# Kernel optimization log

Hardware: AMD Instinct MI355X
Metric: run time of the kernel (lower is better)

Reference implementation:

```python
import jax, jax.numpy as jnp
import numpy as np

DIM = 384
HEADS = 6
DIM_HEAD = 64
INNER = HEADS * DIM_HEAD  # 384


def setup_inputs() -> dict:
    key = jax.random.key(0)
    ks = jax.random.split(key, 6)
    s = 0.02
    return {
        "x_q": jax.random.normal(ks[0], (8, 4096, DIM), dtype=jnp.float32),
        "x_kv": jax.random.normal(ks[1], (8, 4096, DIM), dtype=jnp.float32),
        "Wq": jax.random.normal(ks[2], (DIM, INNER), dtype=jnp.float32) * s,
        "Wkv": jax.random.normal(ks[3], (DIM, 2 * INNER), dtype=jnp.float32) * s,
        "Wout": jax.random.normal(ks[4], (INNER, DIM), dtype=jnp.float32) * s,
        "bout": jax.random.normal(ks[5], (DIM,), dtype=jnp.float32) * s,
    }


def _split_heads(t, b, n):
    # [b, n, h*d] -> [b, h, n, d]
    return t.reshape(b, n, HEADS, DIM_HEAD).transpose(0, 2, 1, 3)


def reference(x_q, x_kv, Wq, Wkv, Wout, bout):
    b, nq, _ = x_q.shape
    nkv = x_kv.shape[1]
    q = x_q @ Wq                      # [b, nq, inner]
    kv_proj = x_kv @ Wkv              # [b, nkv, 2*inner]
    k, v = jnp.split(kv_proj, 2, axis=-1)
    q = _split_heads(q, b, nq)        # [b, h, nq, d]
    k = _split_heads(k, b, nkv)       # [b, h, nkv, d]
    v = _split_heads(v, b, nkv)       # [b, h, nkv, d]
    q = jax.nn.elu(q) + 1.0
    k = jax.nn.elu(k) + 1.0
    kv = jnp.einsum('bhnd,bhnm->bhdm', k, v)             # [b, h, d, d]
    z = 1.0 / (jnp.einsum('bhnd,bhd->bhn', q, k.sum(axis=2)) + 1e-6)
    out = jnp.einsum('bhnd,bhdm->bhnm', q, kv) * z[..., None]  # [b, h, nq, d]
    out = out.transpose(0, 2, 1, 3).reshape(b, nq, INNER)
    return out @ Wout + bout
```

## Files before the change

### kernel.cpp

```cpp
#include <hip/hip_runtime.h>
#include <math.h>

#define BATCH 8
#define SEQ 4096
#define DIMSZ 384
#define HEADS 6
#define DH 64
#define MTOT (BATCH * SEQ)
#define KD 384

typedef short short8 __attribute__((ext_vector_type(8)));
typedef float floatx4 __attribute__((ext_vector_type(4)));
typedef unsigned short ushort4v __attribute__((ext_vector_type(4)));
typedef unsigned short ushort8v __attribute__((ext_vector_type(8)));

__device__ __forceinline__ float elu1(float x) { return x > 0.f ? x + 1.f : __expf(x); }

__device__ __forceinline__ unsigned short f2b(float f) {
    unsigned int u = __float_as_uint(f);
    u = (u + 0x7fffu + ((u >> 16) & 1u)) >> 16;
    return (unsigned short)u;
}
__device__ __forceinline__ float b2f(unsigned short u) {
    return __uint_as_float(((unsigned int)u) << 16);
}

__device__ __forceinline__ void gl16(const void* g, void* l) {
    __builtin_amdgcn_global_load_lds((const __attribute__((address_space(1))) unsigned int*)g,
                                     (__attribute__((address_space(3))) unsigned int*)l, 16, 0, 0);
}

__global__ __launch_bounds__(256) void conv_x2(const float* __restrict__ xq,
                                               const float* __restrict__ xkv,
                                               unsigned short* __restrict__ dq,
                                               unsigned short* __restrict__ dkv) {
    int bx = blockIdx.x;
    const float* src;
    unsigned short* dst;
    if (bx < 6144) { src = xkv; dst = dkv; }
    else { src = xq; dst = dq; bx -= 6144; }
    size_t i = ((size_t)bx * 256 + threadIdx.x) * 8;
    float4 a = *(const float4*)&src[i];
    float4 b = *(const float4*)&src[i + 4];
    ushort8v o;
    o[0] = f2b(a.x); o[1] = f2b(a.y); o[2] = f2b(a.z); o[3] = f2b(a.w);
    o[4] = f2b(b.x); o[5] = f2b(b.y); o[6] = f2b(b.z); o[7] = f2b(b.w);
    *(ushort8v*)&dst[i] = o;
}

__global__ __launch_bounds__(256) void conv_wt3(const float* __restrict__ Wq,
                                                const float* __restrict__ Wkv,
                                                const float* __restrict__ Wout,
                                                unsigned short* __restrict__ WqT,
                                                unsigned short* __restrict__ WkvT,
                                                unsigned short* __restrict__ WoutT) {
    __shared__ float tile[32][33];
    int bx = blockIdx.x;
    const float* W;
    unsigned short* WT;
    int N;
    if (bx < 12) { W = Wq; WT = WqT; N = DIMSZ; }
    else if (bx < 36) { W = Wkv; WT = WkvT; N = 2 * DIMSZ; bx -= 12; }
    else { W = Wout; WT = WoutT; N = DIMSZ; bx -= 36; }
    const int n0 = bx * 32, k0 = blockIdx.y * 32;
    const int tx = threadIdx.x & 31, ty = threadIdx.x >> 5;
#pragma unroll
    for (int i = 0; i < 32; i += 8) tile[ty + i][tx] = W[(size_t)(k0 + ty + i) * N + n0 + tx];
    __syncthreads();
#pragma unroll
    for (int i = 0; i < 32; i += 8)
        WT[(size_t)(n0 + ty + i) * KD + k0 + tx] = f2b(tile[tx][ty + i]);
}

__global__ __launch_bounds__(256, 4) void gemm_kv(const unsigned short* __restrict__ A,
                                                  const unsigned short* __restrict__ WkvT,
                                                  float* __restrict__ pkv,
                                                  float* __restrict__ pks) {
    __shared__ __align__(16) unsigned short buf[17408];
    __shared__ float ksLDS[128];
    unsigned short* As = buf;
    unsigned short* Bs = buf + 8192;
    const int tid = threadIdx.x;
    const int lane = tid & 63, wave = tid >> 6;
    const int l15 = lane & 15, qd = lane >> 4;
    const int fid = blockIdx.x;
    const int xcd = fid & 7;
    const int s = fid >> 3;
    const int h = s % HEADS;
    const int rtl = s / HEADS;
    const int row0 = (xcd * 32 + rtl) * 128;
    const int pidx = (xcd * HEADS + h) * 32 + rtl;
    const int wm = (wave & 1) * 64, wn = (wave >> 1) * 64;

    const unsigned short* Ab = A + (size_t)row0 * KD;
    const unsigned short* Bb = WkvT + (size_t)(h * DH) * KD;
    const int srow = tid >> 3;
    const int scol = (((tid & 7) ^ (srow & 7)) * 8);

    floatx4 zero = {0.f, 0.f, 0.f, 0.f};
    floatx4 acc[4][4];
#pragma unroll
    for (int i = 0; i < 4; ++i)
#pragma unroll
        for (int j = 0; j < 4; ++j) acc[i][j] = zero;

    const int sw = l15 & 7;
    for (int kk = 0; kk < KD; kk += 64) {
        __syncthreads();
#pragma unroll
        for (int i = 0; i < 4; ++i)
            gl16(Ab + (size_t)(i * 32 + srow) * KD + kk + scol, As + i * 2048 + wave * 512);
#pragma unroll
        for (int i = 0; i < 4; ++i)
            gl16(Bb + (size_t)(i * 32 + srow + (i >= 2 ? 320 : 0)) * KD + kk + scol,
                 Bs + i * 2048 + wave * 512);
        __syncthreads();
#pragma unroll
        for (int t = 0; t < 2; ++t) {
            const int chnk = ((t * 4 + qd) ^ sw) * 8;
            short8 af[4], bfr[4];
#pragma unroll
            for (int mi = 0; mi < 4; ++mi)
                af[mi] = *(const short8*)&As[(wm + mi * 16 + l15) * 64 + chnk];
#pragma unroll
            for (int ni = 0; ni < 4; ++ni)
                bfr[ni] = *(const short8*)&Bs[(wn + ni * 16 + l15) * 64 + chnk];
#pragma unroll
            for (int mi = 0; mi < 4; ++mi)
#pragma unroll
                for (int ni = 0; ni < 4; ++ni)
                    acc[mi][ni] = __builtin_amdgcn_mfma_f32_16x16x32_bf16(af[mi], bfr[ni],
                                                                          acc[mi][ni], 0, 0, 0);
        }
    }

    __syncthreads();
    const bool kw = (wn == 0);
    float ksp[4] = {};
#pragma unroll
    for (int mi = 0; mi < 4; ++mi)
#pragma unroll
        for (int ni = 0; ni < 4; ++ni) {
            const int rb = wm + mi * 16 + qd * 4;
            const int cl = wn + ni * 16 + l15;
            ushort4v o;
#pragma unroll
            for (int r = 0; r < 4; ++r) {
                float v = acc[mi][ni][r];
                if (kw) { v = elu1(v); ksp[ni] += v; }
                o[r] = f2b(v);
            }
            *(ushort4v*)&buf[cl * 136 + rb] = o;
        }
    if (kw) {
#pragma unroll
        for (int ni = 0; ni < 4; ++ni) {
            float v = ksp[ni];
            v += __shfl_xor(v, 16);
            v += __shfl_xor(v, 32);
            if (lane < 16) ksLDS[wave * 64 + ni * 16 + lane] = v;
        }
    }
    __syncthreads();
    floatx4 kva[4];
#pragma unroll
    for (int j = 0; j < 4; ++j) kva[j] = zero;
#pragma unroll
    for (int nk = 0; nk < 4; ++nk) {
        short8 afk = *(const short8*)&buf[(wave * 16 + l15) * 136 + nk * 32 + qd * 8];
#pragma unroll
        for (int nj = 0; nj < 4; ++nj) {
            short8 bfv = *(const short8*)&buf[(64 + nj * 16 + l15) * 136 + nk * 32 + qd * 8];
            kva[nj] = __builtin_amdgcn_mfma_f32_16x16x32_bf16(afk, bfv, kva[nj], 0, 0, 0);
        }
    }
    float* P = pkv + (size_t)pidx * 4096;
#pragma unroll
    for (int nj = 0; nj < 4; ++nj)
#pragma unroll
        for (int r = 0; r < 4; ++r)
            __builtin_nontemporal_store(kva[nj][r],
                                        &P[(wave * 16 + qd * 4 + r) * 64 + nj * 16 + l15]);
    if (tid < 64)
        __builtin_nontemporal_store(ksLDS[tid] + ksLDS[64 + tid], &pks[pidx * 64 + tid]);
}

__global__ __launch_bounds__(256) void kv_reduce(const float* __restrict__ pkv,
                                                 const float* __restrict__ pks,
                                                 unsigned short* __restrict__ kv_bf,
                                                 float* __restrict__ ksum_g) {
    const int bh = blockIdx.x;
    const int tid = threadIdx.x;
    unsigned short* kb = kv_bf + (size_t)bh * 4096;
    for (int i0 = tid * 4; i0 < 4096; i0 += 1024) {
        float4 sum = {0.f, 0.f, 0.f, 0.f};
#pragma unroll
        for (int c = 0; c < 32; ++c) {
            float4 p = *(const float4*)&pkv[(size_t)(bh * 32 + c) * 4096 + i0];
            sum.x += p.x; sum.y += p.y; sum.z += p.z; sum.w += p.w;
        }
        const int d = i0 >> 6, m = i0 & 63;
        kb[(m + 0) * 64 + d] = f2b(sum.x);
        kb[(m + 1) * 64 + d] = f2b(sum.y);
        kb[(m + 2) * 64 + d] = f2b(sum.z);
        kb[(m + 3) * 64 + d] = f2b(sum.w);
    }
    if (tid < 64) {
        float sum = 0.f;
#pragma unroll
        for (int c = 0; c < 32; ++c) sum += pks[(bh * 32 + c) * 64 + tid];
        ksum_g[bh * 64 + tid] = sum;
    }
}

__global__ __launch_bounds__(256, 3) void gemm_q_attn(const unsigned short* __restrict__ A,
                                                      const unsigned short* __restrict__ WqT,
                                                      const unsigned short* __restrict__ kv_bf,
                                                      const float* __restrict__ ksum_g,
                                                      unsigned short* __restrict__ attn) {
    __shared__ __align__(16) unsigned short buf[17408];
    __shared__ float ksh[128];
    __shared__ float zsh[256];
    unsigned short* As = buf;
    unsigned short* Bs = buf + 8192;
    const int tid = threadIdx.x;
    const int lane = tid & 63, wave = tid >> 6;
    const int l15 = lane & 15, qd = lane >> 4;
    const int fid = blockIdx.x;
    const int xcd = fid & 7;
    const int s = fid >> 3;
    const int ct = s % 3;
    const int rtl = s / 3;
    const int row0 = (xcd * 32 + rtl) * 128;
    const int col0 = ct * 128;
    const int bh0 = xcd * HEADS + ct * 2;
    const int wd = (wave & 1) * 64, wn2 = (wave >> 1) * 64;

    if (tid < 128) ksh[tid] = ksum_g[bh0 * 64 + tid];

    const unsigned short* Ab = A + (size_t)row0 * KD;
    const unsigned short* Bb = WqT + (size_t)col0 * KD;
    const int srow = tid >> 3;
    const int scol = (((tid & 7) ^ (srow & 7)) * 8);

    floatx4 zero = {0.f, 0.f, 0.f, 0.f};
    floatx4 acc[4][4];
#pragma unroll
    for (int i = 0; i < 4; ++i)
#pragma unroll
        for (int j = 0; j < 4; ++j) acc[i][j] = zero;

    const int sw = l15 & 7;
    for (int kk = 0; kk < KD; kk += 64) {
        __syncthreads();
#pragma unroll
        for (int i = 0; i < 4; ++i)
            gl16(Ab + (size_t)(i * 32 + srow) * KD + kk + scol, As + i * 2048 + wave * 512);
#pragma unroll
        for (int i = 0; i < 4; ++i)
            gl16(Bb + (size_t)(i * 32 + srow) * KD + kk + scol, Bs + i * 2048 + wave * 512);
        __syncthreads();
#pragma unroll
        for (int t = 0; t < 2; ++t) {
            const int chnk = ((t * 4 + qd) ^ sw) * 8;
            short8 wf[4], xf[4];
#pragma unroll
            for (int di = 0; di < 4; ++di)
                wf[di] = *(const short8*)&Bs[(wd + di * 16 + l15) * 64 + chnk];
#pragma unroll
            for (int nj = 0; nj < 4; ++nj)
                xf[nj] = *(const short8*)&As[(wn2 + nj * 16 + l15) * 64 + chnk];
#pragma unroll
            for (int di = 0; di < 4; ++di)
#pragma unroll
                for (int nj = 0; nj < 4; ++nj)
                    acc[di][nj] = __builtin_amdgcn_mfma_f32_16x16x32_bf16(wf[di], xf[nj],
                                                                          acc[di][nj], 0, 0, 0);
        }
    }

    float zp[4] = {};
#pragma unroll
    for (int di = 0; di < 4; ++di)
#pragma unroll
        for (int r = 0; r < 4; ++r) {
            const float ks = ksh[wd + di * 16 + qd * 4 + r];
#pragma unroll
            for (int nj = 0; nj < 4; ++nj) {
                const float q = elu1(acc[di][nj][r]);
                acc[di][nj][r] = q;
                zp[nj] += q * ks;
            }
        }
#pragma unroll
    for (int nj = 0; nj < 4; ++nj) {
        float v = zp[nj];
        v += __shfl_xor(v, 16);
        v += __shfl_xor(v, 32);
        zp[nj] = 1.f / (v + 1e-6f);
    }
    __syncthreads();
    if (lane < 16) {
#pragma unroll
        for (int nj = 0; nj < 4; ++nj) zsh[(wave & 1) * 128 + wn2 + nj * 16 + lane] = zp[nj];
    }
#pragma unroll
    for (int di = 0; di < 4; ++di)
#pragma unroll
        for (int nj = 0; nj < 4; ++nj) {
            const int rb = wd + di * 16 + qd * 4;
            const int cl = wn2 + nj * 16 + l15;
            ushort4v o;
#pragma unroll
            for (int r = 0; r < 4; ++r) o[r] = f2b(acc[di][nj][r]);
            *(ushort4v*)&buf[cl * 136 + rb] = o;
        }
    __syncthreads();
    const int hh = wave & 1;
    const unsigned short* kvB = kv_bf + (size_t)(bh0 + hh) * 4096;
    floatx4 acc2[4][4];
#pragma unroll
    for (int i = 0; i < 4; ++i)
#pragma unroll
        for (int j = 0; j < 4; ++j) acc2[i][j] = zero;
#pragma unroll
    for (int t = 0; t < 2; ++t) {
        short8 bf2[4];
#pragma unroll
        for (int bj = 0; bj < 4; ++bj)
            bf2[bj] = *(const short8*)&kvB[(bj * 16 + l15) * 64 + t * 32 + qd * 8];
#pragma unroll
        for (int ai = 0; ai < 4; ++ai) {
            short8 af =
                *(const short8*)&buf[(wn2 + ai * 16 + l15) * 136 + hh * 64 + t * 32 + qd * 8];
#pragma unroll
            for (int bj = 0; bj < 4; ++bj)
                acc2[ai][bj] =
                    __builtin_amdgcn_mfma_f32_16x16x32_bf16(af, bf2[bj], acc2[ai][bj], 0, 0, 0);
        }
    }
#pragma unroll
    for (int ai = 0; ai < 4; ++ai)
#pragma unroll
        for (int bj = 0; bj < 4; ++bj) {
            const int colg = col0 + hh * 64 + bj * 16 + l15;
#pragma unroll
            for (int r = 0; r < 4; ++r) {
                const int nl = wn2 + ai * 16 + qd * 4 + r;
                const float v = acc2[ai][bj][r] * zsh[hh * 128 + nl];
                attn[(size_t)(row0 + nl) * KD + colg] = f2b(v);
            }
        }
}

__global__ __launch_bounds__(256, 4) void gemm_out(const unsigned short* __restrict__ A,
                                                   const unsigned short* __restrict__ BT,
                                                   float* __restrict__ C,
                                                   const float* __restrict__ bias) {
    __shared__ __align__(16) unsigned short buf[17408];
    unsigned short* As = buf;
    unsigned short* Bs = buf + 8192;
    const int tid = threadIdx.x;
    const int lane = tid & 63, wave = tid >> 6;
    const int l15 = lane & 15, qd = lane >> 4;
    const int fid = blockIdx.x;
    const int xcd = fid & 7;
    const int s = fid >> 3;
    const int row0 = (xcd * 32 + s / 3) * 128;
    const int col0 = (s % 3) * 128;
    const int wm = (wave & 1) * 64, wn = (wave >> 1) * 64;

    const unsigned short* Ab = A + (size_t)row0 * KD;
    const unsigned short* Bb = BT + (size_t)col0 * KD;
    const int srow = tid >> 3;
    const int scol = (((tid & 7) ^ (srow & 7)) * 8);

    floatx4 zero = {0.f, 0.f, 0.f, 0.f};
    floatx4 acc[4][4];
#pragma unroll
    for (int i = 0; i < 4; ++i)
#pragma unroll
        for (int j = 0; j < 4; ++j) acc[i][j] = zero;

    const int sw = l15 & 7;
    for (int kk = 0; kk < KD; kk += 64) {
        __syncthreads();
#pragma unroll
        for (int i = 0; i < 4; ++i)
            gl16(Ab + (size_t)(i * 32 + srow) * KD + kk + scol, As + i * 2048 + wave * 512);
#pragma unroll
        for (int i = 0; i < 4; ++i)
            gl16(Bb + (size_t)(i * 32 + srow) * KD + kk + scol, Bs + i * 2048 + wave * 512);
        __syncthreads();
#pragma unroll
        for (int t = 0; t < 2; ++t) {
            const int chnk = ((t * 4 + qd) ^ sw) * 8;
            short8 af[4], bfr[4];
#pragma unroll
            for (int mi = 0; mi < 4; ++mi)
                af[mi] = *(const short8*)&As[(wm + mi * 16 + l15) * 64 + chnk];
#pragma unroll
            for (int ni = 0; ni < 4; ++ni)
                bfr[ni] = *(const short8*)&Bs[(wn + ni * 16 + l15) * 64 + chnk];
#pragma unroll
            for (int mi = 0; mi < 4; ++mi)
#pragma unroll
                for (int ni = 0; ni < 4; ++ni)
                    acc[mi][ni] = __builtin_amdgcn_mfma_f32_16x16x32_bf16(af[mi], bfr[ni],
                                                                          acc[mi][ni], 0, 0, 0);
        }
    }
#pragma unroll
    for (int mi = 0; mi < 4; ++mi)
#pragma unroll
        for (int ni = 0; ni < 4; ++ni) {
            const int rbase = row0 + wm + mi * 16 + qd * 4;
            const int col = col0 + wn + ni * 16 + l15;
            const float bsv = bias[col];
#pragma unroll
            for (int r = 0; r < 4; ++r)
                __builtin_nontemporal_store(acc[mi][ni][r] + bsv,
                                            &C[(size_t)(rbase + r) * DIMSZ + col]);
        }
}

extern "C" void kernel_launch(void* const* d_in, const int* in_sizes, int n_in,
                              void* d_out, int out_size, void* d_ws, size_t ws_size,
                              hipStream_t stream) {
    const float* x_q = (const float*)d_in[0];
    const float* x_kv = (const float*)d_in[1];
    const float* Wq = (const float*)d_in[2];
    const float* Wkv = (const float*)d_in[3];
    const float* Wout = (const float*)d_in[4];
    const float* bout = (const float*)d_in[5];
    float* out = (float*)d_out;

    char* ws = (char*)d_ws;
    unsigned short* xq_bf = (unsigned short*)(ws + 0);
    unsigned short* xkv_bf = (unsigned short*)(ws + 25165824);
    float* pkv = (float*)(ws + 50331648);
    unsigned short* attn_bf = (unsigned short*)(ws + 50331648);
    unsigned short* WqT = (unsigned short*)(ws + 75497472);
    unsigned short* WkvT = (unsigned short*)(ws + 75792384);
    unsigned short* WoutT = (unsigned short*)(ws + 76382208);
    float* ksum = (float*)(ws + 76677120);
    float* pks = (float*)(ws + 76689408);
    unsigned short* kv_bf = (unsigned short*)(ws + 77082624);

    dim3 blk(256);
    conv_wt3<<<dim3(48, 12), blk, 0, stream>>>(Wq, Wkv, Wout, WqT, WkvT, WoutT);
    conv_x2<<<dim3(12288), blk, 0, stream>>>(x_q, x_kv, xq_bf, xkv_bf);
    gemm_kv<<<dim3(1536), blk, 0, stream>>>(xkv_bf, WkvT, pkv, pks);
    kv_reduce<<<dim3(48), blk, 0, stream>>>(pkv, pks, kv_bf, ksum);
    gemm_q_attn<<<dim3(768), blk, 0, stream>>>(xq_bf, WqT, kv_bf, ksum, attn_bf);
    gemm_out<<<dim3(768), blk, 0, stream>>>(attn_bf, WoutT, out, bout);
}
```

Baseline: 222.1 us.

## Fuse fp32-to-bf16 input conversion into GEMM loads and widen kv_reduce grid

Drops the separate conv_x2 pass. gemm_kv and gemm_q_attn now read fp32 activations directly, convert them to bf16 in registers with the packed v_cvt_pk_bf16_f32 instruction, and write the result into LDS. This removes a full read-and-write pass over both 50MB activation tensors. The trade-off is that gemm_kv re-reads x_kv once per head (6x), the A tile no longer uses async global-to-LDS loads, and the registers hold the fetched data during conversion. kv_reduce is also split over 4x more blocks for parallelism, and the nontemporal stores are replaced with plain stores.

```diff
diff --git a/kernel.cpp b/kernel.cpp
--- a/kernel.cpp
+++ b/kernel.cpp
@@ -13,6 +13,8 @@
 typedef float floatx4 __attribute__((ext_vector_type(4)));
 typedef unsigned short ushort4v __attribute__((ext_vector_type(4)));
 typedef unsigned short ushort8v __attribute__((ext_vector_type(8)));
+typedef unsigned int uint2v __attribute__((ext_vector_type(2)));
+typedef unsigned int uint4v __attribute__((ext_vector_type(4)));
 
 __device__ __forceinline__ float elu1(float x) { return x > 0.f ? x + 1.f : __expf(x); }
 
@@ -24,28 +26,15 @@
 __device__ __forceinline__ float b2f(unsigned short u) {
     return __uint_as_float(((unsigned int)u) << 16);
 }
+__device__ __forceinline__ unsigned int f2b2(float lo, float hi) {
+    unsigned int r;
+    asm("v_cvt_pk_bf16_f32 %0, %1, %2" : "=v"(r) : "v"(lo), "v"(hi));
+    return r;
+}
 
 __device__ __forceinline__ void gl16(const void* g, void* l) {
     __builtin_amdgcn_global_load_lds((const __attribute__((address_space(1))) unsigned int*)g,
                                      (__attribute__((address_space(3))) unsigned int*)l, 16, 0, 0);
-}
-
-__global__ __launch_bounds__(256) void conv_x2(const float* __restrict__ xq,
-                                               const float* __restrict__ xkv,
-                                               unsigned short* __restrict__ dq,
-                                               unsigned short* __restrict__ dkv) {
-    int bx = blockIdx.x;
-    const float* src;
-    unsigned short* dst;
-    if (bx < 6144) { src = xkv; dst = dkv; }
-    else { src = xq; dst = dq; bx -= 6144; }
-    size_t i = ((size_t)bx * 256 + threadIdx.x) * 8;
-    float4 a = *(const float4*)&src[i];
-    float4 b = *(const float4*)&src[i + 4];
-    ushort8v o;
-    o[0] = f2b(a.x); o[1] = f2b(a.y); o[2] = f2b(a.z); o[3] = f2b(a.w);
-    o[4] = f2b(b.x); o[5] = f2b(b.y); o[6] = f2b(b.z); o[7] = f2b(b.w);
-    *(ushort8v*)&dst[i] = o;
 }
 
 __global__ __launch_bounds__(256) void conv_wt3(const float* __restrict__ Wq,
@@ -72,7 +61,7 @@
         WT[(size_t)(n0 + ty + i) * KD + k0 + tx] = f2b(tile[tx][ty + i]);
 }
 
-__global__ __launch_bounds__(256, 4) void gemm_kv(const unsigned short* __restrict__ A,
+__global__ __launch_bounds__(256, 4) void gemm_kv(const float* __restrict__ A,
                                                   const unsigned short* __restrict__ WkvT,
                                                   float* __restrict__ pkv,
                                                   float* __restrict__ pks) {
@@ -92,7 +81,7 @@
     const int pidx = (xcd * HEADS + h) * 32 + rtl;
     const int wm = (wave & 1) * 64, wn = (wave >> 1) * 64;
 
-    const unsigned short* Ab = A + (size_t)row0 * KD;
+    const float* Ab = A + (size_t)row0 * KD;
     const unsigned short* Bb = WkvT + (size_t)(h * DH) * KD;
     const int srow = tid >> 3;
     const int scol = (((tid & 7) ^ (srow & 7)) * 8);
@@ -109,11 +98,24 @@
         __syncthreads();
 #pragma unroll
         for (int i = 0; i < 4; ++i)
-            gl16(Ab + (size_t)(i * 32 + srow) * KD + kk + scol, As + i * 2048 + wave * 512);
-#pragma unroll
-        for (int i = 0; i < 4; ++i)
             gl16(Bb + (size_t)(i * 32 + srow + (i >= 2 ? 320 : 0)) * KD + kk + scol,
                  Bs + i * 2048 + wave * 512);
+        float4 g0[4], g1[4];
+#pragma unroll
+        for (int i = 0; i < 4; ++i) {
+            const float* src = Ab + (size_t)(i * 32 + srow) * KD + kk + scol;
+            g0[i] = *(const float4*)src;
+            g1[i] = *(const float4*)(src + 4);
+        }
+#pragma unroll
+        for (int i = 0; i < 4; ++i) {
+            uint4v u;
+            u[0] = f2b2(g0[i].x, g0[i].y);
+            u[1] = f2b2(g0[i].z, g0[i].w);
+            u[2] = f2b2(g1[i].x, g1[i].y);
+            u[3] = f2b2(g1[i].z, g1[i].w);
+            *(uint4v*)&As[i * 2048 + tid * 8] = u;
+        }
         __syncthreads();
 #pragma unroll
         for (int t = 0; t < 2; ++t) {
@@ -143,14 +145,16 @@
         for (int ni = 0; ni < 4; ++ni) {
             const int rb = wm + mi * 16 + qd * 4;
             const int cl = wn + ni * 16 + l15;
-            ushort4v o;
-#pragma unroll
-            for (int r = 0; r < 4; ++r) {
-                float v = acc[mi][ni][r];
-                if (kw) { v = elu1(v); ksp[ni] += v; }
-                o[r] = f2b(v);
+            float v0 = acc[mi][ni][0], v1 = acc[mi][ni][1];
+            float v2 = acc[mi][ni][2], v3 = acc[mi][ni][3];
+            if (kw) {
+                v0 = elu1(v0); v1 = elu1(v1); v2 = elu1(v2); v3 = elu1(v3);
+                ksp[ni] += (v0 + v1) + (v2 + v3);
             }
-            *(ushort4v*)&buf[cl * 136 + rb] = o;
+            uint2v o;
+            o[0] = f2b2(v0, v1);
+            o[1] = f2b2(v2, v3);
+            *(uint2v*)&buf[cl * 136 + rb] = o;
         }
     if (kw) {
 #pragma unroll
@@ -179,41 +183,38 @@
     for (int nj = 0; nj < 4; ++nj)
 #pragma unroll
         for (int r = 0; r < 4; ++r)
-            __builtin_nontemporal_store(kva[nj][r],
-                                        &P[(wave * 16 + qd * 4 + r) * 64 + nj * 16 + l15]);
-    if (tid < 64)
-        __builtin_nontemporal_store(ksLDS[tid] + ksLDS[64 + tid], &pks[pidx * 64 + tid]);
+            P[(wave * 16 + qd * 4 + r) * 64 + nj * 16 + l15] = kva[nj][r];
+    if (tid < 64) pks[pidx * 64 + tid] = ksLDS[tid] + ksLDS[64 + tid];
 }
 
 __global__ __launch_bounds__(256) void kv_reduce(const float* __restrict__ pkv,
                                                  const float* __restrict__ pks,
                                                  unsigned short* __restrict__ kv_bf,
                                                  float* __restrict__ ksum_g) {
-    const int bh = blockIdx.x;
+    const int bh = blockIdx.x >> 2, dc = blockIdx.x & 3;
     const int tid = threadIdx.x;
     unsigned short* kb = kv_bf + (size_t)bh * 4096;
-    for (int i0 = tid * 4; i0 < 4096; i0 += 1024) {
-        float4 sum = {0.f, 0.f, 0.f, 0.f};
-#pragma unroll
-        for (int c = 0; c < 32; ++c) {
-            float4 p = *(const float4*)&pkv[(size_t)(bh * 32 + c) * 4096 + i0];
-            sum.x += p.x; sum.y += p.y; sum.z += p.z; sum.w += p.w;
-        }
-        const int d = i0 >> 6, m = i0 & 63;
-        kb[(m + 0) * 64 + d] = f2b(sum.x);
-        kb[(m + 1) * 64 + d] = f2b(sum.y);
-        kb[(m + 2) * 64 + d] = f2b(sum.z);
-        kb[(m + 3) * 64 + d] = f2b(sum.w);
-    }
-    if (tid < 64) {
-        float sum = 0.f;
-#pragma unroll
-        for (int c = 0; c < 32; ++c) sum += pks[(bh * 32 + c) * 64 + tid];
-        ksum_g[bh * 64 + tid] = sum;
-    }
-}
-
-__global__ __launch_bounds__(256, 3) void gemm_q_attn(const unsigned short* __restrict__ A,
+    const int i0 = dc * 1024 + tid * 4;
+    float4 sum = {0.f, 0.f, 0.f, 0.f};
+#pragma unroll
+    for (int c = 0; c < 32; ++c) {
+        float4 p = *(const float4*)&pkv[(size_t)(bh * 32 + c) * 4096 + i0];
+        sum.x += p.x; sum.y += p.y; sum.z += p.z; sum.w += p.w;
+    }
+    const int d = i0 >> 6, m = i0 & 63;
+    kb[(m + 0) * 64 + d] = f2b(sum.x);
+    kb[(m + 1) * 64 + d] = f2b(sum.y);
+    kb[(m + 2) * 64 + d] = f2b(sum.z);
+    kb[(m + 3) * 64 + d] = f2b(sum.w);
+    if (dc == 0 && tid < 64) {
+        float s = 0.f;
+#pragma unroll
+        for (int c = 0; c < 32; ++c) s += pks[(bh * 32 + c) * 64 + tid];
+        ksum_g[bh * 64 + tid] = s;
+    }
+}
+
+__global__ __launch_bounds__(256, 3) void gemm_q_attn(const float* __restrict__ A,
                                                       const unsigned short* __restrict__ WqT,
                                                       const unsigned short* __restrict__ kv_bf,
                                                       const float* __restrict__ ksum_g,
@@ -238,7 +239,7 @@
 
     if (tid < 128) ksh[tid] = ksum_g[bh0 * 64 + tid];
 
-    const unsigned short* Ab = A + (size_t)row0 * KD;
+    const float* Ab = A + (size_t)row0 * KD;
     const unsigned short* Bb = WqT + (size_t)col0 * KD;
     const int srow = tid >> 3;
     const int scol = (((tid & 7) ^ (srow & 7)) * 8);
@@ -255,10 +256,23 @@
         __syncthreads();
 #pragma unroll
         for (int i = 0; i < 4; ++i)
-            gl16(Ab + (size_t)(i * 32 + srow) * KD + kk + scol, As + i * 2048 + wave * 512);
-#pragma unroll
-        for (int i = 0; i < 4; ++i)
             gl16(Bb + (size_t)(i * 32 + srow) * KD + kk + scol, Bs + i * 2048 + wave * 512);
+        float4 g0[4], g1[4];
+#pragma unroll
+        for (int i = 0; i < 4; ++i) {
+            const float* src = Ab + (size_t)(i * 32 + srow) * KD + kk + scol;
+            g0[i] = *(const float4*)src;
+            g1[i] = *(const float4*)(src + 4);
+        }
+#pragma unroll
+        for (int i = 0; i < 4; ++i) {
+            uint4v u;
+            u[0] = f2b2(g0[i].x, g0[i].y);
+            u[1] = f2b2(g0[i].z, g0[i].w);
+            u[2] = f2b2(g1[i].x, g1[i].y);
+            u[3] = f2b2(g1[i].z, g1[i].w);
+            *(uint4v*)&As[i * 2048 + tid * 8] = u;
+        }
         __syncthreads();
 #pragma unroll
         for (int t = 0; t < 2; ++t) {
@@ -310,10 +324,10 @@
         for (int nj = 0; nj < 4; ++nj) {
             const int rb = wd + di * 16 + qd * 4;
             const int cl = wn2 + nj * 16 + l15;
-            ushort4v o;
-#pragma unroll
-            for (int r = 0; r < 4; ++r) o[r] = f2b(acc[di][nj][r]);
-            *(ushort4v*)&buf[cl * 136 + rb] = o;
+            uint2v o;
+            o[0] = f2b2(acc[di][nj][0], acc[di][nj][1]);
+            o[1] = f2b2(acc[di][nj][2], acc[di][nj][3]);
+            *(uint2v*)&buf[cl * 136 + rb] = o;
         }
     __syncthreads();
     const int hh = wave & 1;
@@ -436,22 +450,19 @@
     float* out = (float*)d_out;
 
     char* ws = (char*)d_ws;
-    unsigned short* xq_bf = (unsigned short*)(ws + 0);
-    unsigned short* xkv_bf = (unsigned short*)(ws + 25165824);
-    float* pkv = (float*)(ws + 50331648);
-    unsigned short* attn_bf = (unsigned short*)(ws + 50331648);
-    unsigned short* WqT = (unsigned short*)(ws + 75497472);
-    unsigned short* WkvT = (unsigned short*)(ws + 75792384);
-    unsigned short* WoutT = (unsigned short*)(ws + 76382208);
-    float* ksum = (float*)(ws + 76677120);
-    float* pks = (float*)(ws + 76689408);
-    unsigned short* kv_bf = (unsigned short*)(ws + 77082624);
+    float* pkv = (float*)(ws + 0);
+    unsigned short* attn_bf = (unsigned short*)(ws + 0);
+    unsigned short* WqT = (unsigned short*)(ws + 25165824);
+    unsigned short* WkvT = (unsigned short*)(ws + 25460736);
+    unsigned short* WoutT = (unsigned short*)(ws + 26050560);
+    float* ksum = (float*)(ws + 26345472);
+    float* pks = (float*)(ws + 26357760);
+    unsigned short* kv_bf = (unsigned short*)(ws + 26750976);
 
     dim3 blk(256);
     conv_wt3<<<dim3(48, 12), blk, 0, stream>>>(Wq, Wkv, Wout, WqT, WkvT, WoutT);
-    conv_x2<<<dim3(12288), blk, 0, stream>>>(x_q, x_kv, xq_bf, xkv_bf);
-    gemm_kv<<<dim3(1536), blk, 0, stream>>>(xkv_bf, WkvT, pkv, pks);
-    kv_reduce<<<dim3(48), blk, 0, stream>>>(pkv, pks, kv_bf, ksum);
-    gemm_q_attn<<<dim3(768), blk, 0, stream>>>(xq_bf, WqT, kv_bf, ksum, attn_bf);
+    gemm_kv<<<dim3(1536), blk, 0, stream>>>(x_kv, WkvT, pkv, pks);
+    kv_reduce<<<dim3(192), blk, 0, stream>>>(pkv, pks, kv_bf, ksum);
+    gemm_q_attn<<<dim3(768), blk, 0, stream>>>(x_q, WqT, kv_bf, ksum, attn_bf);
     gemm_out<<<dim3(768), blk, 0, stream>>>(attn_bf, WoutT, out, bout);
 }
```

Result: no change. 218.2 us (-1.8%).
